# Kernel optimization log

Hardware: AMD Instinct MI355X
Metric: run time of the kernel (lower is better)

Reference implementation:

```python
import jax, jax.numpy as jnp
import numpy as np

WINDOW_SIZES = (4, 16, 64)
MEMORY_DIM = 256


def setup_inputs() -> dict:
    key = jax.random.key(0)
    ks = jax.random.split(key, 9)
    d_model, mem = 256, MEMORY_DIM
    s_in = 1.0 / np.sqrt(d_model)
    s_mem = 1.0 / np.sqrt(mem)
    return {
        "hidden_states": jax.random.normal(ks[0], (2, 4096, d_model), dtype=jnp.float32),
        # weights stored as (in, out) so projection is x @ W + b
        "Wq": jax.random.normal(ks[1], (d_model, mem), dtype=jnp.float32) * s_in,
        "bq": jax.random.normal(ks[2], (mem,), dtype=jnp.float32) * 0.02,
        "Wk": jax.random.normal(ks[3], (d_model, mem), dtype=jnp.float32) * s_in,
        "bk": jax.random.normal(ks[4], (mem,), dtype=jnp.float32) * 0.02,
        "Wv": jax.random.normal(ks[5], (d_model, mem), dtype=jnp.float32) * s_in,
        "bv": jax.random.normal(ks[6], (mem,), dtype=jnp.float32) * 0.02,
        "Wo": jax.random.normal(ks[7], (mem, d_model), dtype=jnp.float32) * s_mem,
        "bo": jax.random.normal(ks[8], (d_model,), dtype=jnp.float32) * 0.02,
    }


def _gather_patches(h, window):
    # h: (B, L, D). Causal window of `window` positions ending at each l,
    # zero-padded on the left (matches F.pad + unfold in the torch module).
    B, L, D = h.shape
    w = min(window, L)
    padded = jnp.pad(h, ((0, 0), (w - 1, 0), (0, 0)))  # (B, L+w-1, D)
    idx = jnp.arange(L)[:, None] + jnp.arange(w)[None, :]  # (L, w)
    return padded[:, idx]  # (B, L, w, D)


def reference(hidden_states, Wq, bq, Wk, bk, Wv, bv, Wo, bo):
    scale = 1.0 / np.sqrt(MEMORY_DIM)
    q = hidden_states @ Wq + bq  # (B, L, M)
    contexts = []
    for window in WINDOW_SIZES:
        patches = _gather_patches(hidden_states, window)  # (B, L, w, D)
        keys = patches @ Wk + bk      # (B, L, w, M)
        values = patches @ Wv + bv    # (B, L, w, M)
        scores = jnp.einsum('bld,blwd->blw', q, keys) * scale
        attn = jax.nn.softmax(scores, axis=-1)
        contexts.append(jnp.einsum('blw,blwd->bld', attn, values))
    merged = contexts[0]
    for c in contexts[1:]:
        merged = merged + c
    merged = merged / len(contexts)
    return hidden_states + merged @ Wo + bo
```

## Files before the change

kernel.cpp:

```cpp
#include <hip/hip_runtime.h>
#include <hip/hip_bf16.h>

#define D 256
#define NROWS 8192
#define LXK 4160
#define LXV 4176
#define VPAD 64

#define QBLK 16
#define KKEYS 80
#define SSTR 84
#define PSTR 104
#define MSTR 264
#define BSTR 264

typedef unsigned int u32;
typedef unsigned short u16;

typedef short bf16x8 __attribute__((ext_vector_type(8)));
typedef float f32x4 __attribute__((ext_vector_type(4)));

__device__ __forceinline__ u16 f2bf(float f) {
    u32 x = __float_as_uint(f);
    x += 0x7fffu + ((x >> 16) & 1u);
    return (u16)(x >> 16);
}
__device__ __forceinline__ u32 pk2(float a, float b) {
    return (u32)f2bf(a) | ((u32)f2bf(b) << 16);
}

__global__ __launch_bounds__(256) void qkv_mfma(
    const float* __restrict__ H,
    const float* __restrict__ Wq, const float* __restrict__ Wk,
    const float* __restrict__ Wv, const float* __restrict__ Wo,
    const float* __restrict__ bq, const float* __restrict__ bkb,
    const float* __restrict__ bvb,
    u16* __restrict__ Qf, u16* __restrict__ Kx, u16* __restrict__ Vt,
    u16* __restrict__ WoTf)
{
    __shared__ u16 As[64 * 256];
    __shared__ u16 Bs[64 * BSTR];
    __shared__ u16 Eb[64 * 72];

    const int tid = threadIdx.x;
    const int bx = blockIdx.x;
    const int by = blockIdx.y;
    const int mat = bx >> 2;
    const int n0 = (bx & 3) * 64;
    const int row0 = by * 256;
    const int batch = by >> 4;
    const int lrow0 = row0 & 4095;
    const float* __restrict__ W = (mat == 0) ? Wq : (mat == 1) ? Wk : Wv;
    const float* __restrict__ bias = (mat == 0) ? bq : (mat == 1) ? bkb : bvb;

    const int lane = tid & 63, w = tid >> 6;
    const int l15 = lane & 15, lhi = lane >> 4;
    const int rt2 = (w & 1) * 2, ct2 = (w >> 1) * 2;

    {
        const int kp = tid & 31, ng = tid >> 5;
        u32* bd = (u32*)Bs;
        #pragma unroll
        for (int s = 0; s < 4; ++s) {
            const float* wr = W + (size_t)(s * 64 + 2 * kp) * 256 + n0 + ng * 8;
            float4 a0 = *(const float4*)(wr);
            float4 a1 = *(const float4*)(wr + 4);
            float4 b0 = *(const float4*)(wr + 256);
            float4 b1 = *(const float4*)(wr + 260);
            bd[(ng * 8 + 0) * 132 + s * 32 + kp] = pk2(a0.x, b0.x);
            bd[(ng * 8 + 1) * 132 + s * 32 + kp] = pk2(a0.y, b0.y);
            bd[(ng * 8 + 2) * 132 + s * 32 + kp] = pk2(a0.z, b0.z);
            bd[(ng * 8 + 3) * 132 + s * 32 + kp] = pk2(a0.w, b0.w);
            bd[(ng * 8 + 4) * 132 + s * 32 + kp] = pk2(a1.x, b1.x);
            bd[(ng * 8 + 5) * 132 + s * 32 + kp] = pk2(a1.y, b1.y);
            bd[(ng * 8 + 6) * 132 + s * 32 + kp] = pk2(a1.z, b1.z);
            bd[(ng * 8 + 7) * 132 + s * 32 + kp] = pk2(a1.w, b1.w);
        }
    }
    {
        const int r = tid >> 2, cb = (tid & 3) * 64;
        const float* hp = H + (size_t)(row0 + r) * 256 + cb;
        const int swz = (r & 7) << 3;
        #pragma unroll
        for (int i = 0; i < 16; ++i) {
            float4 h4 = *(const float4*)(hp + i * 4);
            uint2 pv; pv.x = pk2(h4.x, h4.y); pv.y = pk2(h4.z, h4.w);
            *(uint2*)(As + ((r * 256 + cb + i * 4) ^ swz)) = pv;
        }
    }
    __syncthreads();

    for (int t = 0; t < 4; ++t) {
        f32x4 acc[2][2];
        #pragma unroll
        for (int rr = 0; rr < 2; ++rr)
            #pragma unroll
            for (int cc = 0; cc < 2; ++cc)
                acc[rr][cc] = (f32x4){0.f, 0.f, 0.f, 0.f};
        #pragma unroll
        for (int rr = 0; rr < 2; ++rr) {
            const int rowa = (rt2 + rr) * 16 + l15;
            const int swa = (rowa & 7) << 3;
            bf16x8 af[8];
            #pragma unroll
            for (int ks = 0; ks < 8; ++ks)
                af[ks] = *(const bf16x8*)(As + ((rowa * 256 + ks * 32 + lhi * 8) ^ swa));
            #pragma unroll
            for (int ks = 0; ks < 8; ++ks)
                #pragma unroll
                for (int cc = 0; cc < 2; ++cc) {
                    bf16x8 bf = *(const bf16x8*)&Bs[((ct2 + cc) * 16 + l15) * BSTR + ks * 32 + lhi * 8];
                    acc[rr][cc] = __builtin_amdgcn_mfma_f32_16x16x32_bf16(af[ks], bf, acc[rr][cc], 0, 0, 0);
                }
        }
        __syncthreads();

        if (mat == 2) {
            #pragma unroll
            for (int cc = 0; cc < 2; ++cc) {
                const int dl = (ct2 + cc) * 16 + l15;
                const float bi = bvb[n0 + dl];
                #pragma unroll
                for (int rr = 0; rr < 2; ++rr)
                    #pragma unroll
                    for (int reg = 0; reg < 4; ++reg)
                        Eb[dl * 72 + (rt2 + rr) * 16 + lhi * 4 + reg] = f2bf(acc[rr][cc][reg] + bi);
            }
        } else {
            #pragma unroll
            for (int cc = 0; cc < 2; ++cc) {
                const int cl = (ct2 + cc) * 16 + l15;
                const float bi = bias[n0 + cl];
                #pragma unroll
                for (int rr = 0; rr < 2; ++rr)
                    #pragma unroll
                    for (int reg = 0; reg < 4; ++reg)
                        Eb[((rt2 + rr) * 16 + lhi * 4 + reg) * 72 + cl] = f2bf(acc[rr][cc][reg] + bi);
            }
        }
        if (t < 3) {
            const int r = tid >> 2, cb = (tid & 3) * 64;
            const float* hp = H + (size_t)(row0 + (t + 1) * 64 + r) * 256 + cb;
            const int swz = (r & 7) << 3;
            #pragma unroll
            for (int i = 0; i < 16; ++i) {
                float4 h4 = *(const float4*)(hp + i * 4);
                uint2 pv; pv.x = pk2(h4.x, h4.y); pv.y = pk2(h4.z, h4.w);
                *(uint2*)(As + ((r * 256 + cb + i * 4) ^ swz)) = pv;
            }
        }
        __syncthreads();

        if (mat == 2) {
            const int d2 = tid >> 2, q = tid & 3;
            uint4 v0 = *(const uint4*)&Eb[d2 * 72 + q * 16];
            uint4 v1 = *(const uint4*)&Eb[d2 * 72 + q * 16 + 8];
            u16* dst = Vt + ((size_t)batch * 256 + n0 + d2) * LXV + VPAD + lrow0 + t * 64 + q * 16;
            *(uint4*)dst = v0;
            *(uint4*)(dst + 8) = v1;
        } else if (mat == 1) {
            const int r2 = tid >> 2, c16 = (tid & 3) * 16;
            uint4 v0 = *(const uint4*)&Eb[r2 * 72 + c16];
            uint4 v1 = *(const uint4*)&Eb[r2 * 72 + c16 + 8];
            u16* dst = Kx + ((size_t)batch * LXK + VPAD + lrow0 + t * 64 + r2) * 256 + n0 + c16;
            *(uint4*)(dst + 0) = v0;
            *(uint4*)(dst + 8) = v1;
        } else {
            const int r2 = tid >> 2, c16 = (tid & 3) * 16;
            const int grow = row0 + t * 64 + r2;
            const int rtile = grow >> 4, rl = grow & 15;
            #pragma unroll
            for (int h = 0; h < 2; ++h) {
                const int gcol = n0 + c16 + h * 8;
                const int ksq = gcol >> 5;
                const int lhq = (gcol >> 3) & 3;
                uint4 v = *(const uint4*)&Eb[r2 * 72 + c16 + h * 8];
                *(uint4*)&Qf[((size_t)rtile * 8 + ksq) * 512 + (rl * 4 + lhq) * 8] = v;
            }
        }
    }

    if (bx == 0 && by < 16) {
        float* Tf = (float*)As;
        const int tr = by >> 2, tc = by & 3;
        __syncthreads();
        {
            const int r = tid >> 2, c0 = (tid & 3) * 16;
            const float* src = Wo + (size_t)(tr * 64 + r) * 256 + tc * 64 + c0;
            #pragma unroll
            for (int i = 0; i < 4; ++i) {
                float4 v = *(const float4*)(src + i * 4);
                Tf[r * 68 + c0 + i * 4 + 0] = v.x;
                Tf[r * 68 + c0 + i * 4 + 1] = v.y;
                Tf[r * 68 + c0 + i * 4 + 2] = v.z;
                Tf[r * 68 + c0 + i * 4 + 3] = v.w;
            }
        }
        __syncthreads();
        {
            const int n = tid >> 2, k0 = (tid & 3) * 16;
            const int gcol = tc * 64 + n;
            const int colt = gcol >> 4, cl = gcol & 15;
            const int gk = tr * 64 + k0;
            const int ksw = gk >> 5;
            const int lhw = (gk >> 3) & 3;
            u32 pw[8];
            #pragma unroll
            for (int i = 0; i < 8; ++i)
                pw[i] = pk2(Tf[(k0 + 2 * i) * 68 + n], Tf[(k0 + 2 * i + 1) * 68 + n]);
            u16* base = WoTf + ((size_t)colt * 8 + ksw) * 512 + (cl * 4 + lhw) * 8;
            *(uint4*)base = *(uint4*)&pw[0];
            *(uint4*)(base + 8) = *(uint4*)&pw[4];
        }
    }
    if (bx == 4 && (by & 15) == 0) {
        const int batch2 = by >> 4;
        const int rowp = tid >> 2, c64 = (tid & 3) * 64;
        u16* dst = Kx + ((size_t)batch2 * LXK + rowp) * 256 + c64;
        #pragma unroll
        for (int j = 0; j < 8; ++j) {
            float4 a = *(const float4*)&bkb[c64 + j * 8];
            float4 b = *(const float4*)&bkb[c64 + j * 8 + 4];
            uint4 o;
            o.x = pk2(a.x, a.y); o.y = pk2(a.z, a.w);
            o.z = pk2(b.x, b.y); o.w = pk2(b.z, b.w);
            *(uint4*)(dst + j * 8) = o;
        }
    }
    if (bx == 8 && (by & 15) == 0) {
        const int batch2 = by >> 4;
        const u16 val = f2bf(bvb[tid]);
        const u32 vv = (u32)val | ((u32)val << 16);
        uint4 o; o.x = vv; o.y = vv; o.z = vv; o.w = vv;
        u16* dst = Vt + ((size_t)batch2 * 256 + tid) * LXV;
        #pragma unroll
        for (int j = 0; j < 8; ++j) *(uint4*)(dst + j * 8) = o;
    }
}

__global__ __launch_bounds__(256) void attn_out(
    const u16* __restrict__ Qf, const u16* __restrict__ Kx,
    const u16* __restrict__ Vt, const u16* __restrict__ WoTf,
    const float* __restrict__ bo, const float* __restrict__ H,
    float* __restrict__ out)
{
    __shared__ __align__(16) char smem[49664];
    u16*  Ks = (u16*)smem;
    u16*  Ml = (u16*)smem;
    float* Sb = (float*)(smem + 40960);
    u16*  Pb = (u16*)(smem + 46336);

    const int tid = threadIdx.x;
    const int lane = tid & 63, w = tid >> 6;
    const int l15 = lane & 15, lhi = lane >> 4;
    const int r0 = blockIdx.x * QBLK;
    const int batch = r0 >> 12;
    const int lb0 = r0 & 4095;
    const size_t kbase = (size_t)batch * LXK + lb0;

    uint4 kreg[10];
    #pragma unroll
    for (int i = 0; i < 10; ++i) {
        const int u = i * 256 + tid;
        const int row = u >> 5, seg = u & 31;
        kreg[i] = *(const uint4*)&Kx[(kbase + row) * 256 + seg * 8];
    }
    #pragma unroll
    for (int i = 0; i < 10; ++i) {
        const int u = i * 256 + tid;
        const int row = u >> 5, seg = u & 31;
        *(uint4*)&Ks[row * 256 + (seg ^ (row & 7)) * 8] = kreg[i];
    }
    __syncthreads();

    const float scale = 0.0625f;
    const u16* qp = Qf + (size_t)(r0 >> 4) * 4096 + (l15 * 4 + lhi) * 8;
    bf16x8 qf[8];
    #pragma unroll
    for (int ks = 0; ks < 8; ++ks) qf[ks] = *(const bf16x8*)(qp + ks * 512);
    for (int T = w; T < 5; T += 4) {
        const int key = T * 16 + l15;
        f32x4 acc = (f32x4){0.f, 0.f, 0.f, 0.f};
        #pragma unroll
        for (int ks = 0; ks < 8; ++ks) {
            bf16x8 kf = *(const bf16x8*)&Ks[key * 256 + ((ks * 4 + lhi) ^ (key & 7)) * 8];
            acc = __builtin_amdgcn_mfma_f32_16x16x32_bf16(qf[ks], kf, acc, 0, 0, 0);
        }
        #pragma unroll
        for (int reg = 0; reg < 4; ++reg)
            Sb[(lhi * 4 + reg) * SSTR + T * 16 + l15] = acc[reg] * scale;
    }
    __syncthreads();

    {
        const int ri = w * 4 + lhi;
        const int jb = l15;
        float s5[5];
        float m = -1e30f;
        #pragma unroll
        for (int c = 0; c < 5; ++c) {
            const int j = jb + 16 * c;
            const float x = Sb[ri * SSTR + j];
            const bool v = (j >= ri + 1) && (j <= ri + 64);
            s5[c] = v ? x : -1e30f;
            m = fmaxf(m, s5[c]);
        }
        #pragma unroll
        for (int o = 1; o < 16; o <<= 1) m = fmaxf(m, __shfl_xor(m, o));
        float e5[5], z64 = 0.f, z16 = 0.f, z4 = 0.f;
        #pragma unroll
        for (int c = 0; c < 5; ++c) {
            const int j = jb + 16 * c;
            const float e = __expf(s5[c] - m);
            e5[c] = e;
            z64 += e;
            if (j >= ri + 49) z16 += e;
            if (j >= ri + 61) z4 += e;
        }
        #pragma unroll
        for (int o = 1; o < 16; o <<= 1) {
            z64 += __shfl_xor(z64, o);
            z16 += __shfl_xor(z16, o);
            z4  += __shfl_xor(z4, o);
        }
        const float i64 = 1.f / z64, i16 = 1.f / z16, i4 = 1.f / z4;
        #pragma unroll
        for (int c = 0; c < 5; ++c) {
            const int j = jb + 16 * c;
            float wt = e5[c] * (i64 + (j >= ri + 49 ? i16 : 0.f) + (j >= ri + 61 ? i4 : 0.f)) * (1.f / 3.f);
            Pb[ri * PSTR + j] = f2bf(wt);
        }
        Pb[ri * PSTR + 80 + jb] = 0;
    }
    __syncthreads();

    bf16x8 pa[3];
    #pragma unroll
    for (int ks = 0; ks < 3; ++ks)
        pa[ks] = *(const bf16x8*)&Pb[l15 * PSTR + ks * 32 + lhi * 8];
    #pragma unroll
    for (int i = 0; i < 4; ++i) {
        const int dt = w * 4 + i;
        const u16* vrow = Vt + ((size_t)batch * 256 + dt * 16 + l15) * LXV + lb0;
        f32x4 acc = (f32x4){0.f, 0.f, 0.f, 0.f};
        #pragma unroll
        for (int ks = 0; ks < 3; ++ks) {
            bf16x8 vb = *(const bf16x8*)(vrow + ks * 32 + lhi * 8);
            acc = __builtin_amdgcn_mfma_f32_16x16x32_bf16(pa[ks], vb, acc, 0, 0, 0);
        }
        #pragma unroll
        for (int reg = 0; reg < 4; ++reg)
            Ml[(lhi * 4 + reg) * MSTR + dt * 16 + l15] = f2bf(acc[reg]);
    }
    __syncthreads();

    bf16x8 afm[8];
    #pragma unroll
    for (int ks = 0; ks < 8; ++ks)
        afm[ks] = *(const bf16x8*)&Ml[l15 * MSTR + ks * 32 + lhi * 8];

    #pragma unroll
    for (int ct = 0; ct < 4; ++ct) {
        const int colt = w * 4 + ct;
        const u16* wrow = WoTf + (size_t)colt * 4096 + (l15 * 4 + lhi) * 8;
        f32x4 oac = (f32x4){0.f, 0.f, 0.f, 0.f};
        #pragma unroll
        for (int ks = 0; ks < 8; ++ks) {
            bf16x8 bf = *(const bf16x8*)(wrow + ks * 512);
            oac = __builtin_amdgcn_mfma_f32_16x16x32_bf16(afm[ks], bf, oac, 0, 0, 0);
        }
        const int col = w * 64 + ct * 16 + l15;
        const float bi = bo[col];
        #pragma unroll
        for (int reg = 0; reg < 4; ++reg) {
            const int r = r0 + lhi * 4 + reg;
            const size_t off = (size_t)r * 256 + col;
            out[off] = H[off] + oac[reg] + bi;
        }
    }
}

extern "C" void kernel_launch(void* const* d_in, const int* in_sizes, int n_in,
                              void* d_out, int out_size, void* d_ws, size_t ws_size,
                              hipStream_t stream) {
    const float* H  = (const float*)d_in[0];
    const float* Wq = (const float*)d_in[1];
    const float* bq = (const float*)d_in[2];
    const float* Wk = (const float*)d_in[3];
    const float* bk = (const float*)d_in[4];
    const float* Wv = (const float*)d_in[5];
    const float* bv = (const float*)d_in[6];
    const float* Wo = (const float*)d_in[7];
    const float* bo = (const float*)d_in[8];
    float* out = (float*)d_out;

    u16* Qf   = (u16*)d_ws;
    u16* Kx   = Qf + (size_t)NROWS * 256;
    u16* Vt   = Kx + (size_t)2 * LXK * 256;
    u16* WoTf = Vt + (size_t)2 * 256 * LXV;

    qkv_mfma<<<dim3(12, 32), 256, 0, stream>>>(H, Wq, Wk, Wv, Wo, bq, bk, bv, Qf, Kx, Vt, WoTf);
    attn_out<<<512, 256, 0, stream>>>(Qf, Kx, Vt, WoTf, bo, H, out);
}
```

Baseline: 47.82 us.

## Store K in MFMA fragment layout and read fragments directly from global

The K projection is now written in the same fragment-tiled layout as Q (16-row tiles, 8 k-slices of 512 elements), including the left padding rows filled with the bias. The attention kernel then loads K fragments straight from global memory into registers for the QK^T MFMAs instead of staging 80 rows into LDS with a swizzle and a barrier. This drops about 40KB of shared memory per block, which should raise occupancy and remove one sync. The cost is that overlapping K tiles get reread from L2 by neighbouring blocks without LDS reuse.

Measured after the change: 47.88 us. Within noise of the previous version (+0.1%).

```diff
diff --git a/kernel.cpp b/kernel.cpp
--- a/kernel.cpp
+++ b/kernel.cpp
@@ -3,12 +3,11 @@
 
 #define D 256
 #define NROWS 8192
-#define LXK 4160
 #define LXV 4176
 #define VPAD 64
+#define KXFB 1064960
 
 #define QBLK 16
-#define KKEYS 80
 #define SSTR 84
 #define PSTR 104
 #define MSTR 264
@@ -35,7 +34,7 @@
     const float* __restrict__ Wv, const float* __restrict__ Wo,
     const float* __restrict__ bq, const float* __restrict__ bkb,
     const float* __restrict__ bvb,
-    u16* __restrict__ Qf, u16* __restrict__ Kx, u16* __restrict__ Vt,
+    u16* __restrict__ Qf, u16* __restrict__ Kxf, u16* __restrict__ Vt,
     u16* __restrict__ WoTf)
 {
     __shared__ u16 As[64 * 256];
@@ -158,24 +157,26 @@
             u16* dst = Vt + ((size_t)batch * 256 + n0 + d2) * LXV + VPAD + lrow0 + t * 64 + q * 16;
             *(uint4*)dst = v0;
             *(uint4*)(dst + 8) = v1;
-        } else if (mat == 1) {
-            const int r2 = tid >> 2, c16 = (tid & 3) * 16;
-            uint4 v0 = *(const uint4*)&Eb[r2 * 72 + c16];
-            uint4 v1 = *(const uint4*)&Eb[r2 * 72 + c16 + 8];
-            u16* dst = Kx + ((size_t)batch * LXK + VPAD + lrow0 + t * 64 + r2) * 256 + n0 + c16;
-            *(uint4*)(dst + 0) = v0;
-            *(uint4*)(dst + 8) = v1;
         } else {
             const int r2 = tid >> 2, c16 = (tid & 3) * 16;
-            const int grow = row0 + t * 64 + r2;
-            const int rtile = grow >> 4, rl = grow & 15;
+            int rtile, rl;
+            u16* base;
+            if (mat == 0) {
+                const int grow = row0 + t * 64 + r2;
+                rtile = grow >> 4; rl = grow & 15;
+                base = Qf;
+            } else {
+                const int prow = VPAD + lrow0 + t * 64 + r2;
+                rtile = prow >> 4; rl = prow & 15;
+                base = Kxf + (size_t)batch * KXFB;
+            }
             #pragma unroll
             for (int h = 0; h < 2; ++h) {
                 const int gcol = n0 + c16 + h * 8;
                 const int ksq = gcol >> 5;
                 const int lhq = (gcol >> 3) & 3;
                 uint4 v = *(const uint4*)&Eb[r2 * 72 + c16 + h * 8];
-                *(uint4*)&Qf[((size_t)rtile * 8 + ksq) * 512 + (rl * 4 + lhq) * 8] = v;
+                *(uint4*)&base[((size_t)rtile * 8 + ksq) * 512 + (rl * 4 + lhq) * 8] = v;
             }
         }
     }
@@ -215,17 +216,14 @@
     }
     if (bx == 4 && (by & 15) == 0) {
         const int batch2 = by >> 4;
-        const int rowp = tid >> 2, c64 = (tid & 3) * 64;
-        u16* dst = Kx + ((size_t)batch2 * LXK + rowp) * 256 + c64;
-        #pragma unroll
-        for (int j = 0; j < 8; ++j) {
-            float4 a = *(const float4*)&bkb[c64 + j * 8];
-            float4 b = *(const float4*)&bkb[c64 + j * 8 + 4];
-            uint4 o;
-            o.x = pk2(a.x, a.y); o.y = pk2(a.z, a.w);
-            o.z = pk2(b.x, b.y); o.w = pk2(b.z, b.w);
-            *(uint4*)(dst + j * 8) = o;
-        }
+        const int ks = tid >> 5, u = tid & 31;
+        const u16 val = f2bf(bkb[ks * 32 + u]);
+        u16* base = Kxf + (size_t)batch2 * KXFB;
+        #pragma unroll
+        for (int pt = 0; pt < 4; ++pt)
+            #pragma unroll
+            for (int rl = 0; rl < 16; ++rl)
+                base[((size_t)pt * 8 + ks) * 512 + rl * 32 + u] = val;
     }
     if (bx == 8 && (by & 15) == 0) {
         const int batch2 = by >> 4;
@@ -239,16 +237,14 @@
 }
 
 __global__ __launch_bounds__(256) void attn_out(
-    const u16* __restrict__ Qf, const u16* __restrict__ Kx,
+    const u16* __restrict__ Qf, const u16* __restrict__ Kxf,
     const u16* __restrict__ Vt, const u16* __restrict__ WoTf,
     const float* __restrict__ bo, const float* __restrict__ H,
     float* __restrict__ out)
 {
-    __shared__ __align__(16) char smem[49664];
-    u16*  Ks = (u16*)smem;
-    u16*  Ml = (u16*)smem;
-    float* Sb = (float*)(smem + 40960);
-    u16*  Pb = (u16*)(smem + 46336);
+    __shared__ float Sb[QBLK * SSTR];
+    __shared__ u16 Pb[QBLK * PSTR];
+    __shared__ u16 Ml[QBLK * MSTR];
 
     const int tid = threadIdx.x;
     const int lane = tid & 63, w = tid >> 6;
@@ -256,34 +252,21 @@
     const int r0 = blockIdx.x * QBLK;
     const int batch = r0 >> 12;
     const int lb0 = r0 & 4095;
-    const size_t kbase = (size_t)batch * LXK + lb0;
-
-    uint4 kreg[10];
-    #pragma unroll
-    for (int i = 0; i < 10; ++i) {
-        const int u = i * 256 + tid;
-        const int row = u >> 5, seg = u & 31;
-        kreg[i] = *(const uint4*)&Kx[(kbase + row) * 256 + seg * 8];
-    }
-    #pragma unroll
-    for (int i = 0; i < 10; ++i) {
-        const int u = i * 256 + tid;
-        const int row = u >> 5, seg = u & 31;
-        *(uint4*)&Ks[row * 256 + (seg ^ (row & 7)) * 8] = kreg[i];
-    }
-    __syncthreads();
 
     const float scale = 0.0625f;
-    const u16* qp = Qf + (size_t)(r0 >> 4) * 4096 + (l15 * 4 + lhi) * 8;
+    const int fidx = (l15 * 4 + lhi) * 8;
+    const u16* qp = Qf + (size_t)(r0 >> 4) * 4096 + fidx;
     bf16x8 qf[8];
     #pragma unroll
     for (int ks = 0; ks < 8; ++ks) qf[ks] = *(const bf16x8*)(qp + ks * 512);
+
+    const u16* kfb = Kxf + (size_t)batch * KXFB + (size_t)(lb0 >> 4) * 4096 + fidx;
     for (int T = w; T < 5; T += 4) {
-        const int key = T * 16 + l15;
+        const u16* kp = kfb + (size_t)T * 4096;
         f32x4 acc = (f32x4){0.f, 0.f, 0.f, 0.f};
         #pragma unroll
         for (int ks = 0; ks < 8; ++ks) {
-            bf16x8 kf = *(const bf16x8*)&Ks[key * 256 + ((ks * 4 + lhi) ^ (key & 7)) * 8];
+            bf16x8 kf = *(const bf16x8*)(kp + ks * 512);
             acc = __builtin_amdgcn_mfma_f32_16x16x32_bf16(qf[ks], kf, acc, 0, 0, 0);
         }
         #pragma unroll
@@ -362,7 +345,7 @@
     #pragma unroll
     for (int ct = 0; ct < 4; ++ct) {
         const int colt = w * 4 + ct;
-        const u16* wrow = WoTf + (size_t)colt * 4096 + (l15 * 4 + lhi) * 8;
+        const u16* wrow = WoTf + (size_t)colt * 4096 + fidx;
         f32x4 oac = (f32x4){0.f, 0.f, 0.f, 0.f};
         #pragma unroll
         for (int ks = 0; ks < 8; ++ks) {
@@ -395,10 +378,10 @@
     float* out = (float*)d_out;
 
     u16* Qf   = (u16*)d_ws;
-    u16* Kx   = Qf + (size_t)NROWS * 256;
-    u16* Vt   = Kx + (size_t)2 * LXK * 256;
+    u16* Kxf  = Qf + (size_t)NROWS * 256;
+    u16* Vt   = Kxf + (size_t)2 * KXFB;
     u16* WoTf = Vt + (size_t)2 * 256 * LXV;
 
-    qkv_mfma<<<dim3(12, 32), 256, 0, stream>>>(H, Wq, Wk, Wv, Wo, bq, bk, bv, Qf, Kx, Vt, WoTf);
-    attn_out<<<512, 256, 0, stream>>>(Qf, Kx, Vt, WoTf, bo, H, out);
-}
+    qkv_mfma<<<dim3(12, 32), 256, 0, stream>>>(H, Wq, Wk, Wv, Wo, bq, bk, bv, Qf, Kxf, Vt, WoTf);
+    attn_out<<<512, 256, 0, stream>>>(Qf, Kxf, Vt, WoTf, bo, H, out);
+}
```
